# Kernel optimization log

Measured on AMD Instinct MI355X. Metric: run time of the kernel, lower is better.

## Reference

```python
import jax, jax.numpy as jnp
import numpy as np
from jax import lax

B, T, IN, H, DIM = 128, 1024, 64, 128, 64


def setup_inputs() -> dict:
    key = jax.random.key(0)
    ks = jax.random.split(key, 14)
    s = 0.05
    return {
        "x": jax.random.normal(ks[0], (B, T, IN), jnp.float32),
        "is_init": jax.random.randint(ks[1], (B, T, 1), 0, 2).astype(bool),
        "hx": jax.random.normal(ks[2], (B, H), jnp.float32),
        # MLP: Linear(IN,128) + ELU, Linear(128,128) + ELU
        "W1": jax.random.normal(ks[3], (128, IN), jnp.float32) * s,
        "b1": jnp.zeros((128,), jnp.float32),
        "W2": jax.random.normal(ks[4], (128, 128), jnp.float32) * s,
        "b2": jnp.zeros((128,), jnp.float32),
        # GRU params (torch layout: [3H, in] with gate order r,z,n)
        "W_ih": jax.random.normal(ks[5], (3 * H, 128), jnp.float32) * s,
        "b_ih": jnp.zeros((3 * H,), jnp.float32),
        "W_hh": jax.random.normal(ks[6], (3 * H, H), jnp.float32) * s,
        "b_hh": jnp.zeros((3 * H,), jnp.float32),
        # output head Linear(128, DIM)
        "W_out": jax.random.normal(ks[7], (DIM, 128), jnp.float32) * s,
        "b_out": jnp.zeros((DIM,), jnp.float32),
    }


def _gru_with_reset(xg, init_mask, h0, W_hh, b_hh):
    # xg: [T,B,3H] precomputed input-side gates; init_mask: [T,B,1] float
    def step(h, inp):
        xg_t, m_t = inp
        h = h * (1.0 - m_t)                       # reset hidden where is_init
        hg = h @ W_hh.T + b_hh                    # [B,3H]
        xr, xz, xn = jnp.split(xg_t, 3, axis=-1)
        hr, hz, hn = jnp.split(hg, 3, axis=-1)
        r = jax.nn.sigmoid(xr + hr)
        z = jax.nn.sigmoid(xz + hz)
        n = jnp.tanh(xn + r * hn)
        h_new = (1.0 - z) * n + z * h
        return h_new, h_new

    hT, ys = lax.scan(step, h0, (xg, init_mask))
    return ys, hT


def reference(x, is_init, hx, W1, b1, W2, b2, W_ih, b_ih, W_hh, b_hh, W_out, b_out):
    # MLP (ELU activations)
    h = jax.nn.elu(x @ W1.T + b1)
    h = jax.nn.elu(h @ W2.T + b2)                 # [B,T,128]
    # precompute input-side gate projections for all timesteps (one big GEMM)
    xg = h @ W_ih.T + b_ih                        # [B,T,3H]
    xg_t = jnp.transpose(xg, (1, 0, 2))           # [T,B,3H]
    m_t = jnp.transpose(is_init.astype(x.dtype), (1, 0, 2))  # [T,B,1]
    ys, hT = _gru_with_reset(xg_t, m_t, hx, W_hh, b_hh)
    y = jnp.transpose(ys, (1, 0, 2))              # [B,T,H]
    out = y @ W_out.T + b_out                     # [B,T,DIM]
    return out, hT
```

## Files before the change

### kernel.cpp

```cpp
#include <hip/hip_runtime.h>


#define T_SZ 1024

typedef __attribute__((ext_vector_type(8))) short short8;
typedef __attribute__((ext_vector_type(4))) float f32x4;
typedef unsigned long long u64;
typedef unsigned int uint32;

__device__ __forceinline__ unsigned short f2b(float f){
  return __builtin_bit_cast(unsigned short, (__bf16)f);
}
__device__ __forceinline__ float b2f(unsigned int hs){
  unsigned int u = hs << 16;
  return __builtin_bit_cast(float, u);
}
__device__ __forceinline__ float rcp_f(float x){ return __builtin_amdgcn_rcpf(x); }
__device__ __forceinline__ float elu(float v){ return v > 0.f ? v : __expf(v) - 1.f; }
__device__ __forceinline__ float sigm(float x){ return rcp_f(1.f + __expf(-x)); }
__device__ __forceinline__ float tanh_fast(float x){
  x = fminf(fmaxf(x, -15.f), 15.f);
  float e = __expf(-2.f * x);
  return (1.f - e) * rcp_f(1.f + e);
}
#define MFMA16(a,b,c) __builtin_amdgcn_mfma_f32_16x16x32_bf16(a, b, c, 0, 0, 0)


__global__ __launch_bounds__(512) void wprep(
    const float* __restrict__ Whh, const float* __restrict__ W1,
    const float* __restrict__ W2,  const float* __restrict__ Wih,
    uint4* __restrict__ wtab)
{
  int rec = blockIdx.x*512 + threadIdx.x;
  if(rec >= 15360) return;
  const float* p;
  if(rec < 6144){
    int q = rec & 3, n_ = (rec >> 2) & 127, ks = (rec >> 9) & 3, gt = rec >> 11;
    p = Whh + (size_t)(n_ + 128*gt)*128 + ks*32 + q*8;
  } else if(rec < 7168){
    int r = rec - 6144;
    int q = r & 3, n_ = (r >> 2) & 127, ks = r >> 9;
    p = W1 + (size_t)n_*64 + ks*32 + q*8;
  } else if(rec < 9216){
    int r = rec - 7168;
    int q = r & 3, n_ = (r >> 2) & 127, ks = r >> 9;
    p = W2 + (size_t)n_*128 + ks*32 + q*8;
  } else {
    int r = rec - 9216;
    int q = r & 3, n_ = (r >> 2) & 127, ks = (r >> 9) & 3, gt = r >> 11;
    p = Wih + (size_t)(n_ + 128*gt)*128 + ks*32 + q*8;
  }
  uint4 o;
  o.x = (uint32)f2b(p[0]) | ((uint32)f2b(p[1]) << 16);
  o.y = (uint32)f2b(p[2]) | ((uint32)f2b(p[3]) << 16);
  o.z = (uint32)f2b(p[4]) | ((uint32)f2b(p[5]) << 16);
  o.w = (uint32)f2b(p[6]) | ((uint32)f2b(p[7]) << 16);
  wtab[rec] = o;
}

__global__ __launch_bounds__(512) void seg_build(const int* __restrict__ ii, uint32* C){
  __shared__ uint32 lh[1024];
  __shared__ uint32 lbase[1024];
  __shared__ uint32 ssum[512];
  __shared__ uint32 sbase;
  uint32* segs = C + 4096;
  const int tid = threadIdx.x;
  const int wv = tid >> 6, lane = tid & 63;
  const int b = blockIdx.x*8 + wv;

  for(int i = tid; i < 1024; i += 512) lh[i] = 0u;
  __syncthreads();

  u64 bal[16], mb[16];
  #pragma unroll
  for(int c=0;c<16;c++){
    int t = c*64 + lane;
    int m = ii[b*T_SZ + t];
    mb[c]  = __ballot(m != 0);
    bal[c] = __ballot((m != 0) || (t == 0));
  }
  int fsA[16]; int nx = T_SZ;
  #pragma unroll
  for(int c=15;c>=0;c--){ fsA[c]=nx; if(bal[c]) nx = c*64 + __builtin_ctzll(bal[c]); }

  int lenA[16], tA[16], rkA[16];
  #pragma unroll
  for(int c=0;c<16;c++){
    lenA[c] = 0;
    if((bal[c] >> lane) & 1ull){
      int t = c*64 + lane;
      u64 hi = (lane < 63) ? (bal[c] >> (lane+1)) : 0ull;
      int nxt = hi ? (t + 1 + __builtin_ctzll(hi)) : fsA[c];
      int len = nxt - t;
      int rst = (int)((mb[c] >> lane) & 1ull);
      len -= rst; t += rst;
      if(len > 0){
        lenA[c] = len; tA[c] = t;
        rkA[c] = (int)atomicAdd(&lh[1024 - len], 1u);
      }
    }
  }
  __syncthreads();

  uint32 c0 = lh[2*tid], c1 = lh[2*tid+1];
  ssum[tid] = c0 + c1;
  __syncthreads();
  #pragma unroll
  for(int off=1; off<512; off<<=1){
    uint32 v = (tid >= off) ? ssum[tid-off] : 0u;
    __syncthreads();
    ssum[tid] += v;
    __syncthreads();
  }
  uint32 excl = tid ? ssum[tid-1] : 0u;
  lbase[2*tid]   = excl;
  lbase[2*tid+1] = excl + c0;
  uint32 total = ssum[511];
  uint32 padded = (total + 15u) & ~15u;
  if(tid == 0){
    sbase = atomicAdd(&C[2], padded);
    atomicAdd(&C[1], padded >> 4);
  }
  __syncthreads();
  const uint32 base = sbase;

  #pragma unroll
  for(int c=0;c<16;c++){
    if(lenA[c] > 0){
      uint32 slot = base + lbase[1024 - lenA[c]] + (uint32)rkA[c];
      segs[slot] = ((uint32)b << 21) | ((uint32)tA[c] << 11) | (uint32)lenA[c];
    }
  }
  for(uint32 i = total + tid; i < padded; i += 512) segs[base + i] = 0u;
}

__global__ __launch_bounds__(512) void mlp2(
    const float* __restrict__ x,
    const uint4* __restrict__ wtab,
    const float* __restrict__ b1, const float* __restrict__ b2,
    unsigned short* __restrict__ h2)
{
  __shared__ __align__(16) char smem[35840];
  unsigned short* xs  = (unsigned short*)smem;
  unsigned short* h1l = (unsigned short*)(smem + 18432);
  const int tid = threadIdx.x;
  const int wv = tid >> 6, l = tid & 63, quad = l >> 4, col = l & 15;
  const int n = 16*wv + col;

  short8 w1f[2], w2f[4];
  #pragma unroll
  for(int ks=0; ks<2; ks++)
    w1f[ks] = __builtin_bit_cast(short8, wtab[6144 + (ks*128 + n)*4 + quad]);
  #pragma unroll
  for(int ks=0; ks<4; ks++)
    w2f[ks] = __builtin_bit_cast(short8, wtab[7168 + (ks*128 + n)*4 + quad]);
  const float b1v = b1[n], b2v = b2[n];

  const int srow = tid >> 5, sk = tid & 31;

  for(int tile = blockIdx.x; tile < 2048; tile += gridDim.x){
    const int g = tile & 7, t0 = (tile >> 3) * 4;
    {
      const float* src = x + (size_t)(16*g + srow)*(T_SZ*64) + (size_t)t0*64;
      #pragma unroll
      for(int j=0; j<2; j++){
        int s = sk + 32*j;
        float4 v = ((const float4*)src)[s];
        int tt = s >> 4, k = (s & 15) * 4;
        unsigned short* dst = xs + (tt*16 + srow)*72 + k;
        dst[0]=f2b(v.x); dst[1]=f2b(v.y); dst[2]=f2b(v.z); dst[3]=f2b(v.w);
      }
    }
    __syncthreads();
    #pragma unroll
    for(int tt=0; tt<4; tt++){
      f32x4 acc = {b1v, b1v, b1v, b1v};
      #pragma unroll
      for(int ks=0; ks<2; ks++){
        short8 a = *(const short8*)&xs[(tt*16 + col)*72 + ks*32 + quad*8];
        acc = MFMA16(a, w1f[ks], acc);
      }
      #pragma unroll
      for(int r=0; r<4; r++)
        h1l[(tt*16 + quad*4 + r)*136 + n] = f2b(elu(acc[r]));
    }
    __syncthreads();
    #pragma unroll
    for(int tt=0; tt<4; tt++){
      f32x4 acc = {b2v, b2v, b2v, b2v};
      #pragma unroll
      for(int ks=0; ks<4; ks++){
        short8 a = *(const short8*)&h1l[(tt*16 + col)*136 + ks*32 + quad*8];
        acc = MFMA16(a, w2f[ks], acc);
      }
      const int t = t0 + tt;
      #pragma unroll
      for(int r=0; r<4; r++){
        int row = quad*4 + r;
        h2[((size_t)(t*8 + g)*16 + row)*128 + n] = f2b(elu(acc[r]));
      }
    }
  }
}

__global__ __launch_bounds__(512) void xgproj(
    const unsigned short* h2, const int* __restrict__ ii,
    const uint4* __restrict__ wtab,
    const float* __restrict__ bih, const float* __restrict__ bhh,
    unsigned short* __restrict__ xg, unsigned short* ys,
    float* __restrict__ hT)
{
  __shared__ __align__(16) unsigned short h2l[4*16*136];
  __shared__ int iil[64];
  const int tid = threadIdx.x;
  const int wv = tid >> 6, l = tid & 63, quad = l >> 4, col = l & 15;
  const int n = 16*wv + col;

  short8 wif[3][4];
  #pragma unroll
  for(int gt=0; gt<3; gt++){
    #pragma unroll
    for(int ks=0; ks<4; ks++)
      wif[gt][ks] = __builtin_bit_cast(short8, wtab[9216 + ((gt*4 + ks)*128 + n)*4 + quad]);
  }
  float bihv[3], bhhv[3];
  #pragma unroll
  for(int gt=0; gt<3; gt++){ bihv[gt] = bih[n + 128*gt]; bhhv[gt] = bhh[n + 128*gt]; }

  for(int tile = blockIdx.x; tile < 2048; tile += gridDim.x){
    const int g = tile & 7, t0 = (tile >> 3) * 4;
    {
      const int w = tid >> 3, j = tid & 7;
      const int tt = w >> 4, row = w & 15;
      const unsigned short* src = h2 + ((size_t)((t0 + tt)*8 + g)*16 + row)*128 + j*16;
      unsigned short* dst = &h2l[(tt*16 + row)*136 + j*16];
      #pragma unroll
      for(int i2=0; i2<4; i2++)
        *(u64*)(dst + i2*4) = *(const u64*)(src + i2*4);
    }
    if(tid < 64) iil[tid] = ii[(16*g + (tid & 15))*T_SZ + t0 + (tid >> 4)];
    __syncthreads();

    uint32 xgo[4];
    #pragma unroll
    for(int r=0; r<4; r++)
      xgo[r] = (((uint32)(16*g + quad*4 + r) << 10) + (uint32)t0) * 384u + (uint32)n;
    #pragma unroll
    for(int tt=0; tt<4; tt++){
      f32x4 a0 = {bihv[0], bihv[0], bihv[0], bihv[0]};
      f32x4 a1 = {bihv[1], bihv[1], bihv[1], bihv[1]};
      f32x4 a2 = {bihv[2], bihv[2], bihv[2], bihv[2]};
      #pragma unroll
      for(int ks=0; ks<4; ks++){
        short8 a = *(const short8*)&h2l[(tt*16 + col)*136 + ks*32 + quad*8];
        a0 = MFMA16(a, wif[0][ks], a0);
        a1 = MFMA16(a, wif[1][ks], a1);
        a2 = MFMA16(a, wif[2][ks], a2);
      }
      const int t = t0 + tt;
      #pragma unroll
      for(int r=0; r<4; r++){
        int row = quad*4 + r;
        if(iil[tt*16 + row] != 0){
          float rr = sigm(a0[r] + bhhv[0]);
          float zz = sigm(a1[r] + bhhv[1]);
          float nn = tanh_fast(a2[r] + rr*bhhv[2]);
          float h1 = (1.f - zz)*nn;
          ys[((size_t)(t*8 + g)*16 + row)*128 + n] = f2b(h1);
          if(t == T_SZ-1)
            hT[(16*g + row)*128 + n] = h1;
        } else {
          unsigned short* p = xg + xgo[r] + (uint32)(tt*384);
          p[0]   = f2b(a0[r]);
          p[128] = f2b(a1[r]);
          p[256] = f2b(a2[r]);
        }
      }
    }
    __syncthreads();
  }
}

__global__ __launch_bounds__(512) void gru_seg_scan(
    const unsigned short* __restrict__ xg,
    const float* __restrict__ hx,
    const uint4* __restrict__ wbf, const float* __restrict__ bhh,
    const uint32* __restrict__ C,
    unsigned short* __restrict__ ys, float* __restrict__ hT)
{
  __shared__ unsigned short hl[2][16*136];
  __shared__ unsigned short xbuf[2][16*388];
  __shared__ int srb[16], srt[16], srlen[16];
  const uint32 ntile = C[1];
  const uint32 tile = blockIdx.x;
  if(tile >= ntile) return;

  const int tid = threadIdx.x;
  const int wv = tid >> 6, l = tid & 63, quad = l >> 4, col = l & 15;
  const int nidx = 16*wv + col;
  const int frow = tid >> 5, fk = tid & 31;
  const uint32* segs = C + 4096;

  short8 whf[3][4];
  float bhv[3];
  #pragma unroll
  for(int gt=0; gt<3; gt++){
    bhv[gt] = bhh[nidx + 128*gt];
    #pragma unroll
    for(int ks=0; ks<4; ks++){
      uint4 w = wbf[((gt*4 + ks)*128 + nidx)*4 + quad];
      whf[gt][ks] = __builtin_bit_cast(short8, w);
    }
  }

  if(tid < 16){
    uint32 w = segs[16*tile + (uint32)tid];
    srb[tid] = (int)(w >> 21);
    srt[tid] = (int)((w >> 11) & 1023u);
    srlen[tid] = (int)(w & 2047u);
  }
  __syncthreads();
  const int maxlen = srlen[0];
  const int fb = srb[frow], ft = srt[frow], fl = srlen[frow];

  float hreg[4];
  #pragma unroll
  for(int r=0; r<4; r++){
    int row = quad*4 + r;
    int b = srb[row], t0 = srt[row];
    float h0 = 0.f;
    if(srlen[row] > 0){
      h0 = (t0 == 0) ? hx[b*128 + nidx]
                     : b2f(ys[((size_t)((t0-1)*8 + (b>>4))*16 + (b&15))*128 + nidx]);
    }
    hreg[r] = h0;
    hl[0][row*136 + nidx] = f2b(h0);
  }
  {
    const unsigned short* src = xg + ((size_t)fb*T_SZ + ft)*384;
    unsigned short* xb = &xbuf[0][frow*388];
    #pragma unroll
    for(int i2=0; i2<3; i2++)
      *(u64*)(xb + i2*128 + fk*4) = *(const u64*)(src + i2*128 + fk*4);
  }

  int cur = 0;
  for(int i=0; i<maxlen; i++){
    __syncthreads();
    short8 af[4];
    #pragma unroll
    for(int ks=0; ks<4; ks++)
      af[ks] = *(const short8*)&hl[cur][col*136 + ks*32 + quad*8];
    f32x4 ar = {bhv[0], bhv[0], bhv[0], bhv[0]};
    f32x4 az = {bhv[1], bhv[1], bhv[1], bhv[1]};
    f32x4 an = {bhv[2], bhv[2], bhv[2], bhv[2]};
    #pragma unroll
    for(int ks=0; ks<4; ks++){
      ar = MFMA16(af[ks], whf[0][ks], ar);
      az = MFMA16(af[ks], whf[1][ks], az);
      an = MFMA16(af[ks], whf[2][ks], an);
    }
    u64 p0, p1, p2;
    {
      int tc = (i+1 < fl) ? i+1 : (fl > 0 ? fl-1 : 0);
      const unsigned short* src = xg + ((size_t)fb*T_SZ + (ft + tc))*384;
      p0 = *(const u64*)(src +       fk*4);
      p1 = *(const u64*)(src + 128 + fk*4);
      p2 = *(const u64*)(src + 256 + fk*4);
    }
    if(i >= 1 && i <= fl){
      int t = ft + i - 1;
      u64 hv = *(const u64*)&hl[cur][frow*136 + fk*4];
      *(u64*)(ys + ((size_t)(t*8 + (fb>>4))*16 + (fb&15))*128 + fk*4) = hv;
      if(i == fl && ft + fl == T_SZ){
        #pragma unroll
        for(int j=0; j<4; j++)
          hT[fb*128 + fk*4 + j] = b2f(hl[cur][frow*136 + fk*4 + j]);
      }
    }
    const unsigned short* xb = &xbuf[cur][0];
    #pragma unroll
    for(int r=0; r<4; r++){
      int row = quad*4 + r;
      float xrv = b2f(xb[row*388 +       nidx]);
      float xzv = b2f(xb[row*388 + 128 + nidx]);
      float xnv = b2f(xb[row*388 + 256 + nidx]);
      float rr = sigm(xrv + ar[r]);
      float zz = sigm(xzv + az[r]);
      float nn = tanh_fast(xnv + rr*an[r]);
      float hnew = (1.f - zz)*nn + zz*hreg[r];
      hreg[r] = hnew;
      hl[cur^1][row*136 + nidx] = f2b(hnew);
    }
    {
      unsigned short* xb2 = &xbuf[cur^1][frow*388];
      *(u64*)(xb2 +       fk*4) = p0;
      *(u64*)(xb2 + 128 + fk*4) = p1;
      *(u64*)(xb2 + 256 + fk*4) = p2;
    }
    cur ^= 1;
  }
  __syncthreads();
  if(maxlen >= 1 && fl == maxlen){
    int t = ft + maxlen - 1;
    u64 hv = *(const u64*)&hl[cur][frow*136 + fk*4];
    *(u64*)(ys + ((size_t)(t*8 + (fb>>4))*16 + (fb&15))*128 + fk*4) = hv;
    if(ft + fl == T_SZ){
      #pragma unroll
      for(int j=0; j<4; j++)
        hT[fb*128 + fk*4 + j] = b2f(hl[cur][frow*136 + fk*4 + j]);
    }
  }
}

__global__ __launch_bounds__(256) void out_gemm(
    const unsigned short* __restrict__ ys,
    const float* __restrict__ Wout, const float* __restrict__ bout,
    float* __restrict__ outp)
{
  const int tid = threadIdx.x;
  const int wv = tid >> 6, l = tid & 63, quad = l >> 4, col = l & 15;
  const int n = 16*wv + col;
  short8 wof[4];
  #pragma unroll
  for(int ks=0; ks<4; ks++){
    const float* p = Wout + n*128 + ks*32 + quad*8;
    const float4* q = (const float4*)p;
    float4 u0 = q[0], u1 = q[1];
    short8 v;
    v[0]=(short)f2b(u0.x); v[1]=(short)f2b(u0.y); v[2]=(short)f2b(u0.z); v[3]=(short)f2b(u0.w);
    v[4]=(short)f2b(u1.x); v[5]=(short)f2b(u1.y); v[6]=(short)f2b(u1.z); v[7]=(short)f2b(u1.w);
    wof[ks] = v;
  }
  const float bov = bout[n];
  for(int tile = blockIdx.x; tile < 8192; tile += gridDim.x){
    const int t = tile >> 3, g = tile & 7;
    const unsigned short* yt = ys + (size_t)tile * 16 * 128;
    f32x4 acc = {bov, bov, bov, bov};
    #pragma unroll
    for(int ks=0; ks<4; ks++){
      short8 a = *(const short8*)&yt[col*128 + ks*32 + quad*8];
      acc = MFMA16(a, wof[ks], acc);
    }
    #pragma unroll
    for(int r=0; r<4; r++)
      outp[(size_t)(16*g + quad*4 + r)*(T_SZ*64) + (size_t)t*64 + n] = acc[r];
  }
}

extern "C" void kernel_launch(void* const* d_in, const int* in_sizes, int n_in,
                              void* d_out, int out_size, void* d_ws, size_t ws_size,
                              hipStream_t stream)
{
  const float* x    = (const float*)d_in[0];
  const int*   ii   = (const int*)  d_in[1];
  const float* hx   = (const float*)d_in[2];
  const float* W1   = (const float*)d_in[3];
  const float* b1   = (const float*)d_in[4];
  const float* W2   = (const float*)d_in[5];
  const float* b2   = (const float*)d_in[6];
  const float* Wih  = (const float*)d_in[7];
  const float* bih  = (const float*)d_in[8];
  const float* Whh  = (const float*)d_in[9];
  const float* bhh  = (const float*)d_in[10];
  const float* Wout = (const float*)d_in[11];
  const float* bout = (const float*)d_in[12];

  float* outp = (float*)d_out;
  float* hT   = outp + (size_t)128 * T_SZ * 64;
  uint32* C   = (uint32*)d_out;
  uint4* wtab = (uint4*)((char*)d_out + (1u<<20));

  unsigned short* xg = (unsigned short*)d_ws;
  unsigned short* ys = (unsigned short*)((char*)d_ws + 100663296ull);

  hipMemsetAsync(C, 0, 64, stream);
  wprep      <<<dim3(30),   dim3(512),  0, stream>>>(Whh, W1, W2, Wih, wtab);
  seg_build  <<<dim3(16),   dim3(512),  0, stream>>>(ii, C);
  mlp2       <<<dim3(2048), dim3(512),  0, stream>>>(x, wtab, b1, b2, ys);
  xgproj     <<<dim3(2048), dim3(512),  0, stream>>>(ys, ii, wtab, bih, bhh, xg, ys, hT);
  gru_seg_scan<<<dim3(4160),dim3(512),  0, stream>>>(xg, hx, wtab, bhh, C, ys, hT);
  out_gemm   <<<dim3(2048), dim3(256),  0, stream>>>(ys, Wout, bout, outp);
}
```

Measured before the change: 225.4 us.

## Merge prep kernels, double-buffer xgproj tiles, shrink grids, raise MFMA priority

The weight-prep and segment-build kernels become one launch with blockIdx-based dispatch, removing a launch. xgproj now runs a persistent loop that prefetches the next tile's h2 rows and reset flags into registers while the current tile computes, then writes them into a second shared buffer. The mlp2 and xgproj grids are reduced so each block handles several tiles, and mlp2 gains a barrier at the end of each iteration. The GRU scan raises wave priority around its MFMA block. These changes add register pressure and double the shared memory in xgproj.

```diff
diff --git a/kernel.cpp b/kernel.cpp
--- a/kernel.cpp
+++ b/kernel.cpp
@@ -26,112 +26,112 @@
 #define MFMA16(a,b,c) __builtin_amdgcn_mfma_f32_16x16x32_bf16(a, b, c, 0, 0, 0)
 
 
-__global__ __launch_bounds__(512) void wprep(
+__global__ __launch_bounds__(512) void prep(
     const float* __restrict__ Whh, const float* __restrict__ W1,
     const float* __restrict__ W2,  const float* __restrict__ Wih,
-    uint4* __restrict__ wtab)
+    uint4* __restrict__ wtab, const int* __restrict__ ii, uint32* C)
 {
-  int rec = blockIdx.x*512 + threadIdx.x;
-  if(rec >= 15360) return;
-  const float* p;
-  if(rec < 6144){
-    int q = rec & 3, n_ = (rec >> 2) & 127, ks = (rec >> 9) & 3, gt = rec >> 11;
-    p = Whh + (size_t)(n_ + 128*gt)*128 + ks*32 + q*8;
-  } else if(rec < 7168){
-    int r = rec - 6144;
-    int q = r & 3, n_ = (r >> 2) & 127, ks = r >> 9;
-    p = W1 + (size_t)n_*64 + ks*32 + q*8;
-  } else if(rec < 9216){
-    int r = rec - 7168;
-    int q = r & 3, n_ = (r >> 2) & 127, ks = r >> 9;
-    p = W2 + (size_t)n_*128 + ks*32 + q*8;
+  if(blockIdx.x < 30){
+    int rec = blockIdx.x*512 + threadIdx.x;
+    if(rec >= 15360) return;
+    const float* p;
+    if(rec < 6144){
+      int q = rec & 3, n_ = (rec >> 2) & 127, ks = (rec >> 9) & 3, gt = rec >> 11;
+      p = Whh + (size_t)(n_ + 128*gt)*128 + ks*32 + q*8;
+    } else if(rec < 7168){
+      int r = rec - 6144;
+      int q = r & 3, n_ = (r >> 2) & 127, ks = r >> 9;
+      p = W1 + (size_t)n_*64 + ks*32 + q*8;
+    } else if(rec < 9216){
+      int r = rec - 7168;
+      int q = r & 3, n_ = (r >> 2) & 127, ks = r >> 9;
+      p = W2 + (size_t)n_*128 + ks*32 + q*8;
+    } else {
+      int r = rec - 9216;
+      int q = r & 3, n_ = (r >> 2) & 127, ks = (r >> 9) & 3, gt = r >> 11;
+      p = Wih + (size_t)(n_ + 128*gt)*128 + ks*32 + q*8;
+    }
+    uint4 o;
+    o.x = (uint32)f2b(p[0]) | ((uint32)f2b(p[1]) << 16);
+    o.y = (uint32)f2b(p[2]) | ((uint32)f2b(p[3]) << 16);
+    o.z = (uint32)f2b(p[4]) | ((uint32)f2b(p[5]) << 16);
+    o.w = (uint32)f2b(p[6]) | ((uint32)f2b(p[7]) << 16);
+    wtab[rec] = o;
   } else {
-    int r = rec - 9216;
-    int q = r & 3, n_ = (r >> 2) & 127, ks = (r >> 9) & 3, gt = r >> 11;
-    p = Wih + (size_t)(n_ + 128*gt)*128 + ks*32 + q*8;
-  }
-  uint4 o;
-  o.x = (uint32)f2b(p[0]) | ((uint32)f2b(p[1]) << 16);
-  o.y = (uint32)f2b(p[2]) | ((uint32)f2b(p[3]) << 16);
-  o.z = (uint32)f2b(p[4]) | ((uint32)f2b(p[5]) << 16);
-  o.w = (uint32)f2b(p[6]) | ((uint32)f2b(p[7]) << 16);
-  wtab[rec] = o;
-}
-
-__global__ __launch_bounds__(512) void seg_build(const int* __restrict__ ii, uint32* C){
-  __shared__ uint32 lh[1024];
-  __shared__ uint32 lbase[1024];
-  __shared__ uint32 ssum[512];
-  __shared__ uint32 sbase;
-  uint32* segs = C + 4096;
-  const int tid = threadIdx.x;
-  const int wv = tid >> 6, lane = tid & 63;
-  const int b = blockIdx.x*8 + wv;
-
-  for(int i = tid; i < 1024; i += 512) lh[i] = 0u;
-  __syncthreads();
-
-  u64 bal[16], mb[16];
-  #pragma unroll
-  for(int c=0;c<16;c++){
-    int t = c*64 + lane;
-    int m = ii[b*T_SZ + t];
-    mb[c]  = __ballot(m != 0);
-    bal[c] = __ballot((m != 0) || (t == 0));
-  }
-  int fsA[16]; int nx = T_SZ;
-  #pragma unroll
-  for(int c=15;c>=0;c--){ fsA[c]=nx; if(bal[c]) nx = c*64 + __builtin_ctzll(bal[c]); }
-
-  int lenA[16], tA[16], rkA[16];
-  #pragma unroll
-  for(int c=0;c<16;c++){
-    lenA[c] = 0;
-    if((bal[c] >> lane) & 1ull){
+    __shared__ uint32 lh[1024];
+    __shared__ uint32 lbase[1024];
+    __shared__ uint32 ssum[512];
+    __shared__ uint32 sbase;
+    uint32* segs = C + 4096;
+    const int tid = threadIdx.x;
+    const int wv = tid >> 6, lane = tid & 63;
+    const int b = (blockIdx.x - 30)*8 + wv;
+
+    for(int i = tid; i < 1024; i += 512) lh[i] = 0u;
+    __syncthreads();
+
+    u64 bal[16], mb[16];
+    #pragma unroll
+    for(int c=0;c<16;c++){
       int t = c*64 + lane;
-      u64 hi = (lane < 63) ? (bal[c] >> (lane+1)) : 0ull;
-      int nxt = hi ? (t + 1 + __builtin_ctzll(hi)) : fsA[c];
-      int len = nxt - t;
-      int rst = (int)((mb[c] >> lane) & 1ull);
-      len -= rst; t += rst;
-      if(len > 0){
-        lenA[c] = len; tA[c] = t;
-        rkA[c] = (int)atomicAdd(&lh[1024 - len], 1u);
-      }
-    }
-  }
-  __syncthreads();
-
-  uint32 c0 = lh[2*tid], c1 = lh[2*tid+1];
-  ssum[tid] = c0 + c1;
-  __syncthreads();
-  #pragma unroll
-  for(int off=1; off<512; off<<=1){
-    uint32 v = (tid >= off) ? ssum[tid-off] : 0u;
-    __syncthreads();
-    ssum[tid] += v;
-    __syncthreads();
-  }
-  uint32 excl = tid ? ssum[tid-1] : 0u;
-  lbase[2*tid]   = excl;
-  lbase[2*tid+1] = excl + c0;
-  uint32 total = ssum[511];
-  uint32 padded = (total + 15u) & ~15u;
-  if(tid == 0){
-    sbase = atomicAdd(&C[2], padded);
-    atomicAdd(&C[1], padded >> 4);
-  }
-  __syncthreads();
-  const uint32 base = sbase;
-
-  #pragma unroll
-  for(int c=0;c<16;c++){
-    if(lenA[c] > 0){
-      uint32 slot = base + lbase[1024 - lenA[c]] + (uint32)rkA[c];
-      segs[slot] = ((uint32)b << 21) | ((uint32)tA[c] << 11) | (uint32)lenA[c];
-    }
-  }
-  for(uint32 i = total + tid; i < padded; i += 512) segs[base + i] = 0u;
+      int m = ii[b*T_SZ + t];
+      mb[c]  = __ballot(m != 0);
+      bal[c] = __ballot((m != 0) || (t == 0));
+    }
+    int fsA[16]; int nx = T_SZ;
+    #pragma unroll
+    for(int c=15;c>=0;c--){ fsA[c]=nx; if(bal[c]) nx = c*64 + __builtin_ctzll(bal[c]); }
+
+    int lenA[16], tA[16], rkA[16];
+    #pragma unroll
+    for(int c=0;c<16;c++){
+      lenA[c] = 0;
+      if((bal[c] >> lane) & 1ull){
+        int t = c*64 + lane;
+        u64 hi = (lane < 63) ? (bal[c] >> (lane+1)) : 0ull;
+        int nxt = hi ? (t + 1 + __builtin_ctzll(hi)) : fsA[c];
+        int len = nxt - t;
+        int rst = (int)((mb[c] >> lane) & 1ull);
+        len -= rst; t += rst;
+        if(len > 0){
+          lenA[c] = len; tA[c] = t;
+          rkA[c] = (int)atomicAdd(&lh[1024 - len], 1u);
+        }
+      }
+    }
+    __syncthreads();
+
+    uint32 c0 = lh[2*tid], c1 = lh[2*tid+1];
+    ssum[tid] = c0 + c1;
+    __syncthreads();
+    #pragma unroll
+    for(int off=1; off<512; off<<=1){
+      uint32 v = (tid >= off) ? ssum[tid-off] : 0u;
+      __syncthreads();
+      ssum[tid] += v;
+      __syncthreads();
+    }
+    uint32 excl = tid ? ssum[tid-1] : 0u;
+    lbase[2*tid]   = excl;
+    lbase[2*tid+1] = excl + c0;
+    uint32 total = ssum[511];
+    uint32 padded = (total + 15u) & ~15u;
+    if(tid == 0){
+      sbase = atomicAdd(&C[2], padded);
+      atomicAdd(&C[1], padded >> 4);
+    }
+    __syncthreads();
+    const uint32 base = sbase;
+
+    #pragma unroll
+    for(int c=0;c<16;c++){
+      if(lenA[c] > 0){
+        uint32 slot = base + lbase[1024 - lenA[c]] + (uint32)rkA[c];
+        segs[slot] = ((uint32)b << 21) | ((uint32)tA[c] << 11) | (uint32)lenA[c];
+      }
+    }
+    for(uint32 i = total + tid; i < padded; i += 512) segs[base + i] = 0u;
+  }
 }
 
 __global__ __launch_bounds__(512) void mlp2(
@@ -200,6 +200,7 @@
         h2[((size_t)(t*8 + g)*16 + row)*128 + n] = f2b(elu(acc[r]));
       }
     }
+    __syncthreads();
   }
 }
 
@@ -210,8 +211,8 @@
     unsigned short* __restrict__ xg, unsigned short* ys,
     float* __restrict__ hT)
 {
-  __shared__ __align__(16) unsigned short h2l[4*16*136];
-  __shared__ int iil[64];
+  __shared__ __align__(16) unsigned short h2l[2][4*16*136];
+  __shared__ int iil[2][64];
   const int tid = threadIdx.x;
   const int wv = tid >> 6, l = tid & 63, quad = l >> 4, col = l & 15;
   const int n = 16*wv + col;
@@ -227,57 +228,79 @@
   #pragma unroll
   for(int gt=0; gt<3; gt++){ bihv[gt] = bih[n + 128*gt]; bhhv[gt] = bhh[n + 128*gt]; }
 
-  for(int tile = blockIdx.x; tile < 2048; tile += gridDim.x){
+  const int w = tid >> 3, j = tid & 7;
+  const int stt = w >> 4, srow2 = w & 15;
+
+  int tile = blockIdx.x;
+  {
     const int g = tile & 7, t0 = (tile >> 3) * 4;
+    const unsigned short* src = h2 + ((size_t)((t0 + stt)*8 + g)*16 + srow2)*128 + j*16;
+    unsigned short* dst = &h2l[0][(stt*16 + srow2)*136 + j*16];
+    #pragma unroll
+    for(int i2=0; i2<4; i2++)
+      *(u64*)(dst + i2*4) = *(const u64*)(src + i2*4);
+    if(tid < 64) iil[0][tid] = ii[(16*g + (tid & 15))*T_SZ + t0 + (tid >> 4)];
+  }
+  __syncthreads();
+
+  int p = 0;
+  while(tile < 2048){
+    const int ntile = tile + (int)gridDim.x;
+    u64 r0=0, r1=0, r2=0, r3=0; int iv = 0;
+    if(ntile < 2048){
+      const int g = ntile & 7, t0 = (ntile >> 3) * 4;
+      const unsigned short* src = h2 + ((size_t)((t0 + stt)*8 + g)*16 + srow2)*128 + j*16;
+      r0 = ((const u64*)src)[0]; r1 = ((const u64*)src)[1];
+      r2 = ((const u64*)src)[2]; r3 = ((const u64*)src)[3];
+      if(tid < 64) iv = ii[(16*g + (tid & 15))*T_SZ + t0 + (tid >> 4)];
+    }
     {
-      const int w = tid >> 3, j = tid & 7;
-      const int tt = w >> 4, row = w & 15;
-      const unsigned short* src = h2 + ((size_t)((t0 + tt)*8 + g)*16 + row)*128 + j*16;
-      unsigned short* dst = &h2l[(tt*16 + row)*136 + j*16];
-      #pragma unroll
-      for(int i2=0; i2<4; i2++)
-        *(u64*)(dst + i2*4) = *(const u64*)(src + i2*4);
-    }
-    if(tid < 64) iil[tid] = ii[(16*g + (tid & 15))*T_SZ + t0 + (tid >> 4)];
-    __syncthreads();
-
-    uint32 xgo[4];
-    #pragma unroll
-    for(int r=0; r<4; r++)
-      xgo[r] = (((uint32)(16*g + quad*4 + r) << 10) + (uint32)t0) * 384u + (uint32)n;
-    #pragma unroll
-    for(int tt=0; tt<4; tt++){
-      f32x4 a0 = {bihv[0], bihv[0], bihv[0], bihv[0]};
-      f32x4 a1 = {bihv[1], bihv[1], bihv[1], bihv[1]};
-      f32x4 a2 = {bihv[2], bihv[2], bihv[2], bihv[2]};
-      #pragma unroll
-      for(int ks=0; ks<4; ks++){
-        short8 a = *(const short8*)&h2l[(tt*16 + col)*136 + ks*32 + quad*8];
-        a0 = MFMA16(a, wif[0][ks], a0);
-        a1 = MFMA16(a, wif[1][ks], a1);
-        a2 = MFMA16(a, wif[2][ks], a2);
-      }
-      const int t = t0 + tt;
-      #pragma unroll
-      for(int r=0; r<4; r++){
-        int row = quad*4 + r;
-        if(iil[tt*16 + row] != 0){
-          float rr = sigm(a0[r] + bhhv[0]);
-          float zz = sigm(a1[r] + bhhv[1]);
-          float nn = tanh_fast(a2[r] + rr*bhhv[2]);
-          float h1 = (1.f - zz)*nn;
-          ys[((size_t)(t*8 + g)*16 + row)*128 + n] = f2b(h1);
-          if(t == T_SZ-1)
-            hT[(16*g + row)*128 + n] = h1;
-        } else {
-          unsigned short* p = xg + xgo[r] + (uint32)(tt*384);
-          p[0]   = f2b(a0[r]);
-          p[128] = f2b(a1[r]);
-          p[256] = f2b(a2[r]);
+      const int g = tile & 7, t0 = (tile >> 3) * 4;
+      uint32 xgo[4];
+      #pragma unroll
+      for(int r=0; r<4; r++)
+        xgo[r] = (((uint32)(16*g + quad*4 + r) << 10) + (uint32)t0) * 384u + (uint32)n;
+      #pragma unroll
+      for(int tt=0; tt<4; tt++){
+        f32x4 a0 = {bihv[0], bihv[0], bihv[0], bihv[0]};
+        f32x4 a1 = {bihv[1], bihv[1], bihv[1], bihv[1]};
+        f32x4 a2 = {bihv[2], bihv[2], bihv[2], bihv[2]};
+        #pragma unroll
+        for(int ks=0; ks<4; ks++){
+          short8 a = *(const short8*)&h2l[p][(tt*16 + col)*136 + ks*32 + quad*8];
+          a0 = MFMA16(a, wif[0][ks], a0);
+          a1 = MFMA16(a, wif[1][ks], a1);
+          a2 = MFMA16(a, wif[2][ks], a2);
         }
-      }
-    }
-    __syncthreads();
+        const int t = t0 + tt;
+        #pragma unroll
+        for(int r=0; r<4; r++){
+          int row = quad*4 + r;
+          if(iil[p][tt*16 + row] != 0){
+            float rr = sigm(a0[r] + bhhv[0]);
+            float zz = sigm(a1[r] + bhhv[1]);
+            float nn = tanh_fast(a2[r] + rr*bhhv[2]);
+            float h1 = (1.f - zz)*nn;
+            ys[((size_t)(t*8 + g)*16 + row)*128 + n] = f2b(h1);
+            if(t == T_SZ-1)
+              hT[(16*g + row)*128 + n] = h1;
+          } else {
+            unsigned short* pp = xg + xgo[r] + (uint32)(tt*384);
+            pp[0]   = f2b(a0[r]);
+            pp[128] = f2b(a1[r]);
+            pp[256] = f2b(a2[r]);
+          }
+        }
+      }
+    }
+    if(ntile < 2048){
+      unsigned short* dst = &h2l[p^1][(stt*16 + srow2)*136 + j*16];
+      *(u64*)(dst     ) = r0; *(u64*)(dst +  4) = r1;
+      *(u64*)(dst +  8) = r2; *(u64*)(dst + 12) = r3;
+      if(tid < 64) iil[p^1][tid] = iv;
+    }
+    __syncthreads();
+    tile = ntile; p ^= 1;
   }
 }
 
@@ -347,6 +370,7 @@
   int cur = 0;
   for(int i=0; i<maxlen; i++){
     __syncthreads();
+    __builtin_amdgcn_s_setprio(1);
     short8 af[4];
     #pragma unroll
     for(int ks=0; ks<4; ks++)
@@ -360,6 +384,7 @@
       az = MFMA16(af[ks], whf[1][ks], az);
       an = MFMA16(af[ks], whf[2][ks], an);
     }
+    __builtin_amdgcn_s_setprio(0);
     u64 p0, p1, p2;
     {
       int tc = (i+1 < fl) ? i+1 : (fl > 0 ? fl-1 : 0);
@@ -475,10 +500,9 @@
   unsigned short* ys = (unsigned short*)((char*)d_ws + 100663296ull);
 
   hipMemsetAsync(C, 0, 64, stream);
-  wprep      <<<dim3(30),   dim3(512),  0, stream>>>(Whh, W1, W2, Wih, wtab);
-  seg_build  <<<dim3(16),   dim3(512),  0, stream>>>(ii, C);
-  mlp2       <<<dim3(2048), dim3(512),  0, stream>>>(x, wtab, b1, b2, ys);
-  xgproj     <<<dim3(2048), dim3(512),  0, stream>>>(ys, ii, wtab, bih, bhh, xg, ys, hT);
+  prep       <<<dim3(46),   dim3(512),  0, stream>>>(Whh, W1, W2, Wih, wtab, ii, C);
+  mlp2       <<<dim3(1024), dim3(512),  0, stream>>>(x, wtab, b1, b2, ys);
+  xgproj     <<<dim3(512),  dim3(512),  0, stream>>>(ys, ii, wtab, bih, bhh, xg, ys, hT);
   gru_seg_scan<<<dim3(4160),dim3(512),  0, stream>>>(xg, hx, wtab, bhh, C, ys, hT);
   out_gemm   <<<dim3(2048), dim3(256),  0, stream>>>(ys, Wout, bout, outp);
 }
```

New measurement: 217.7 us. -3.4%, faster.
